# Performance work log

Measured on AMD Instinct MI355X. Metric: run time of the kernel, lower is better.

The kernel has to match this reference:

```python
import jax, jax.numpy as jnp
import numpy as np
from jax import lax

EPS = 1e-5

def conv4d(x, w, stride=1, padding=0):
    # x: [N, C, X, Y, Z, W4]; w: [O, I, kx, ky, kz, kw]
    dn = lax.conv_dimension_numbers(x.shape, w.shape, ('NCXYZW', 'OIXYZW', 'NCXYZW'))
    return lax.conv_general_dilated(x, w, window_strides=(stride,) * 4,
                                    padding=[(padding, padding)] * 4,
                                    dimension_numbers=dn)

def groupnorm1(x, w, b):
    # GroupNorm(num_groups=1): normalize over channel + all spatial dims per sample
    mu = jnp.mean(x, axis=(1, 2, 3, 4, 5), keepdims=True)
    var = jnp.mean(jnp.square(x - mu), axis=(1, 2, 3, 4, 5), keepdims=True)
    xn = (x - mu) * lax.rsqrt(var + EPS)
    shape = (1, -1, 1, 1, 1, 1)
    return xn * w.reshape(shape) + b.reshape(shape)

def setup_inputs() -> dict:
    key = jax.random.key(0)
    ks = jax.random.split(key, 16)
    inp, oup, hidden, se_dim = 32, 32, 128, 8  # hidden = inp*4, se_dim = int(inp*0.25)
    B, S = 1, 16
    sc1 = 1.0 / np.sqrt(inp)
    sc3 = 1.0 / np.sqrt(hidden * 81)
    scp = 1.0 / np.sqrt(hidden)
    return {
        'x': jax.random.normal(ks[0], (B, inp, S, S, S, S), dtype=jnp.float32),
        'g0_w': jnp.ones((inp,), jnp.float32),
        'g0_b': jnp.zeros((inp,), jnp.float32),
        'w1': jax.random.normal(ks[1], (hidden, inp, 1, 1, 1, 1), jnp.float32) * sc1,
        'gn1_w': jnp.ones((hidden,), jnp.float32),
        'gn1_b': jnp.zeros((hidden,), jnp.float32),
        'w2': jax.random.normal(ks[2], (hidden, hidden, 3, 3, 3, 3), jnp.float32) * sc3,
        'gn2_w': jnp.ones((hidden,), jnp.float32),
        'gn2_b': jnp.zeros((hidden,), jnp.float32),
        'se_w1': jax.random.normal(ks[3], (se_dim, hidden), jnp.float32) * scp,
        'se_w2': jax.random.normal(ks[4], (hidden, se_dim), jnp.float32) / np.sqrt(se_dim),
        'w3': jax.random.normal(ks[5], (oup, hidden, 1, 1, 1, 1), jnp.float32) * scp,
        'gn3_w': jnp.ones((oup,), jnp.float32),
        'gn3_b': jnp.zeros((oup,), jnp.float32),
    }

def reference(x, g0_w, g0_b, w1, gn1_w, gn1_b, w2, gn2_w, gn2_b, se_w1, se_w2, w3, gn3_w, gn3_b):
    # PreNorm
    h = groupnorm1(x, g0_w, g0_b)
    # expand 1^4 conv + GN + GELU
    h = conv4d(h, w1)
    h = jax.nn.gelu(groupnorm1(h, gn1_w, gn1_b), approximate=False)
    # 3^4 conv, pad 1 + GN + GELU
    h = conv4d(h, w2, padding=1)
    h = jax.nn.gelu(groupnorm1(h, gn2_w, gn2_b), approximate=False)
    # SE: squeeze over 4 spatial dims, Linear -> GELU -> Linear -> sigmoid, scale
    y = jnp.mean(h, axis=(2, 3, 4, 5))                      # [B, hidden]
    y = jax.nn.gelu(y @ se_w1.T, approximate=False) @ se_w2.T
    y = jax.nn.sigmoid(y)[:, :, None, None, None, None]
    h = h * y
    # project 1^4 conv + GN
    h = conv4d(h, w3)
    return groupnorm1(h, gn3_w, gn3_b)
```

## Files before the change

kernel.cpp:

```cpp
#include <hip/hip_runtime.h>
#include <hip/hip_bf16.h>
#include <math.h>

typedef __hip_bfloat16 bf16;
typedef short bf16x8 __attribute__((ext_vector_type(8)));
typedef float f32x4 __attribute__((ext_vector_type(4)));

#define EPSV 1e-5f

__device__ __forceinline__ float gelu_exact(float x) {
    return 0.5f * x * (1.0f + erff(x * 0.70710678118654752f));
}

__device__ __forceinline__ void block_reduce2(float& a, float& b, float* sm) {
    #pragma unroll
    for (int off = 32; off > 0; off >>= 1) {
        a += __shfl_down(a, off);
        b += __shfl_down(b, off);
    }
    int lane = threadIdx.x & 63, wid = threadIdx.x >> 6;
    int nw = blockDim.x >> 6;
    if (lane == 0) { sm[wid*2] = a; sm[wid*2+1] = b; }
    __syncthreads();
    if (threadIdx.x == 0) {
        for (int i = 1; i < nw; ++i) { a += sm[i*2]; b += sm[i*2+1]; }
    }
}

__device__ __forceinline__ unsigned pk_bf2(float lo, float hi) {
    union { __hip_bfloat162 b2; unsigned u; } cv;
    cv.b2 = __float22bfloat162_rn(make_float2(lo, hi));
    return cv.u;
}

__device__ __forceinline__ void gload_lds16(const void* g, void* l) {
    __builtin_amdgcn_global_load_lds(
        (const __attribute__((address_space(1))) void*)g,
        (__attribute__((address_space(3))) void*)l, 16, 0, 0);
}

__global__ __launch_bounds__(256) void k0_stats_x(const float* __restrict__ x,
                                                  float* __restrict__ stats) {
    __shared__ float sm[16];
    const float4* x4 = (const float4*)x;
    int idx = blockIdx.x * 256 + threadIdx.x;
    float s = 0.f, q = 0.f;
    for (int i = idx; i < (1 << 19); i += gridDim.x * 256) {
        float4 v = x4[i];
        s += v.x + v.y + v.z + v.w;
        q += v.x*v.x + v.y*v.y + v.z*v.z + v.w*v.w;
    }
    block_reduce2(s, q, sm);
    if (threadIdx.x == 0) { atomicAdd(&stats[0], s); atomicAdd(&stats[1], q); }
}

__global__ __launch_bounds__(256) void kw_transpose(const float* __restrict__ w2,
                                                    bf16* __restrict__ wt2) {
    int idx = blockIdx.x * 256 + threadIdx.x;
    if (idx >= 81 * 128 * 128) return;
    int tap = idx >> 14;
    int r = idx & 16383;
    int o = r >> 7;
    int ci = r & 127;
    wt2[idx] = __float2bfloat16(w2[(o * 128 + ci) * 81 + tap]);
}

__global__ __launch_bounds__(256) void k1_conv1(
    const float* __restrict__ x, const float* __restrict__ w1,
    const float* __restrict__ g0w, const float* __restrict__ g0b,
    float* __restrict__ h1, float* __restrict__ stats)
{
    __shared__ float We[128 * 32];
    __shared__ float Be[128];
    __shared__ float sm[16];
    float mu = stats[0] * (1.f / 2097152.f);
    float var = stats[1] * (1.f / 2097152.f) - mu * mu;
    float rs = rsqrtf(var + EPSV);
    int t = threadIdx.x;
    for (int i = t; i < 128 * 32; i += 256) {
        int ci = i & 31;
        We[i] = w1[i] * g0w[ci] * rs;
    }
    if (t < 128) {
        float acc = 0.f;
        for (int ci = 0; ci < 32; ++ci)
            acc += w1[t * 32 + ci] * (g0b[ci] - mu * rs * g0w[ci]);
        Be[t] = acc;
    }
    __syncthreads();
    int s = blockIdx.x * 256 + t;
    float xv[32];
    #pragma unroll
    for (int ci = 0; ci < 32; ++ci) xv[ci] = x[ci * 65536 + s];
    float lsum = 0.f, lsq = 0.f;
    for (int o = 0; o < 128; ++o) {
        float acc = Be[o];
        const float4* wr = (const float4*)&We[o * 32];
        #pragma unroll
        for (int c4 = 0; c4 < 8; ++c4) {
            float4 w = wr[c4];
            acc += w.x * xv[c4*4] + w.y * xv[c4*4+1] + w.z * xv[c4*4+2] + w.w * xv[c4*4+3];
        }
        h1[o * 65536 + s] = acc;
        lsum += acc; lsq += acc * acc;
    }
    block_reduce2(lsum, lsq, sm);
    if (t == 0) { atomicAdd(&stats[2], lsum); atomicAdd(&stats[3], lsq); }
}

__global__ __launch_bounds__(256) void k2_gn1_pad(
    const float* __restrict__ h1, bf16* __restrict__ P, const float* __restrict__ stats,
    const float* __restrict__ gw, const float* __restrict__ gb)
{
    __shared__ float tile[128 * 65];
    float mu = stats[2] * (1.f / 8388608.f);
    float var = stats[3] * (1.f / 8388608.f) - mu * mu;
    float rs = rsqrtf(var + EPSV);
    int t = threadIdx.x;
    int sbase = blockIdx.x * 64;
    for (int p = 0; p < 32; ++p) {
        int idx = p * 256 + t;
        int ci = idx >> 6, sl = idx & 63;
        float v = h1[ci * 65536 + sbase + sl];
        v = (v - mu) * rs * gw[ci] + gb[ci];
        tile[ci * 65 + sl] = gelu_exact(v);
    }
    __syncthreads();
    for (int p = 0; p < 4; ++p) {
        int idx = p * 256 + t;
        int r = idx >> 4, cg = idx & 15;
        int s = sbase + r;
        int w = s & 15, z = (s >> 4) & 15, y = (s >> 8) & 15, xx = s >> 12;
        int prow = (((xx + 1) * 18 + y + 1) * 18 + z + 1) * 18 + w + 1;
        int c0 = cg * 8;
        uint4 u;
        u.x = pk_bf2(tile[(c0+0)*65 + r], tile[(c0+1)*65 + r]);
        u.y = pk_bf2(tile[(c0+2)*65 + r], tile[(c0+3)*65 + r]);
        u.z = pk_bf2(tile[(c0+4)*65 + r], tile[(c0+5)*65 + r]);
        u.w = pk_bf2(tile[(c0+6)*65 + r], tile[(c0+7)*65 + r]);
        *(uint4*)((char*)P + ((size_t)prow * 256 + c0 * 2)) = u;
    }
}

__global__ __launch_bounds__(256) void k3_conv2(
    const bf16* __restrict__ P, const bf16* __restrict__ wt2,
    float* __restrict__ h2, float* __restrict__ stats)
{
    __shared__ __align__(16) short As[23040];
    __shared__ __align__(16) short Ws[16384];
    __shared__ float sm[16];
    int t = threadIdx.x;
    int lane = t & 63, ww = t >> 6;
    int lo = lane & 15, hi = lane >> 4;
    int b = blockIdx.x;
    int X = b >> 5, Y = (b >> 1) & 15, Z0 = (b & 1) * 8;
    int zg = ww >> 1, og = ww & 1;

    int wbase[4], wxor[4];
    #pragma unroll
    for (int n = 0; n < 4; ++n) {
        int row = og * 64 + n * 16 + lo;
        wbase[n] = row << 8;
        wxor[n] = (row & 7) << 4;
    }

    f32x4 acc[4][4];
    #pragma unroll
    for (int m = 0; m < 4; ++m)
        #pragma unroll
        for (int n = 0; n < 4; ++n) acc[m][n] = (f32x4){0.f, 0.f, 0.f, 0.f};

    const char* Pb = (const char*)P;
    const char* Wb = (const char*)wt2;

    for (int kxy = 0; kxy < 9; ++kxy) {
        int kx = kxy / 3, ky = kxy - kx * 3;
        __syncthreads();
        int rowstart = ((X + kx) * 18 + (Y + ky)) * 324 + Z0 * 18;
        const char* gA = Pb + (size_t)rowstart * 256;
        for (int c = ww; c < 45; c += 4) {
            int L = c * 1024 + lane * 16;
            int srcoff = L ^ (((L >> 8) & 7) << 4);
            gload_lds16(gA + srcoff, (char*)As + c * 1024);
        }
        for (int t9 = 0; t9 < 9; ++t9) {
            int kz = t9 / 3, kw = t9 - kz * 3;
            int tap = kxy * 9 + t9;
            __syncthreads();
            const char* gW = Wb + (size_t)tap * 32768;
            for (int c = ww; c < 32; c += 4) {
                int L = c * 1024 + lane * 16;
                int srcoff = L ^ (((L >> 8) & 7) << 4);
                gload_lds16(gW + srcoff, (char*)Ws + c * 1024);
            }
            int abase[4], axor[4];
            #pragma unroll
            for (int m = 0; m < 4; ++m) {
                int row = (zg * 4 + m + kz) * 18 + lo + kw;
                abase[m] = row << 8;
                axor[m] = (row & 7) << 4;
            }
            __syncthreads();
            #pragma unroll
            for (int kk = 0; kk < 4; ++kk) {
                int cb = kk * 64 + hi * 16;
                bf16x8 a[4], bb[4];
                #pragma unroll
                for (int m = 0; m < 4; ++m)
                    a[m] = *(const bf16x8*)((const char*)As + abase[m] + (cb ^ axor[m]));
                #pragma unroll
                for (int n = 0; n < 4; ++n)
                    bb[n] = *(const bf16x8*)((const char*)Ws + wbase[n] + (cb ^ wxor[n]));
                #pragma unroll
                for (int m = 0; m < 4; ++m)
                    #pragma unroll
                    for (int n = 0; n < 4; ++n)
                        acc[m][n] = __builtin_amdgcn_mfma_f32_16x16x32_bf16(
                            a[m], bb[n], acc[m][n], 0, 0, 0);
            }
        }
    }

    float ls = 0.f, lq = 0.f;
    int sXY = (X * 16 + Y) * 16;
    #pragma unroll
    for (int m = 0; m < 4; ++m) {
        int z = Z0 + zg * 4 + m;
        int s = (sXY + z) * 16 + hi * 4;
        #pragma unroll
        for (int n = 0; n < 4; ++n) {
            int o = og * 64 + n * 16 + lo;
            *(f32x4*)(h2 + (size_t)o * 65536 + s) = acc[m][n];
            #pragma unroll
            for (int e = 0; e < 4; ++e) { float v = acc[m][n][e]; ls += v; lq += v * v; }
        }
    }
    __syncthreads();
    block_reduce2(ls, lq, sm);
    if (t == 0) { atomicAdd(&stats[4], ls); atomicAdd(&stats[5], lq); }
}

__global__ __launch_bounds__(256) void k4_gn2_se(
    float* __restrict__ h2, const float* __restrict__ stats,
    const float* __restrict__ gw, const float* __restrict__ gb,
    float* __restrict__ chansum)
{
    __shared__ float sm[4];
    float mu = stats[4] * (1.f / 8388608.f);
    float var = stats[5] * (1.f / 8388608.f) - mu * mu;
    float rs = rsqrtf(var + EPSV);
    int chan = blockIdx.x >> 4, seg = blockIdx.x & 15;
    float w = gw[chan], bb = gb[chan];
    float lsum = 0.f;
    int base = chan * 65536 + seg * 4096;
    for (int k = 0; k < 16; ++k) {
        int i = base + k * 256 + threadIdx.x;
        float v = gelu_exact((h2[i] - mu) * rs * w + bb);
        h2[i] = v;
        lsum += v;
    }
    #pragma unroll
    for (int off = 32; off > 0; off >>= 1) lsum += __shfl_down(lsum, off);
    int lane = threadIdx.x & 63, wid = threadIdx.x >> 6;
    if (lane == 0) sm[wid] = lsum;
    __syncthreads();
    if (threadIdx.x == 0) atomicAdd(&chansum[chan], sm[0] + sm[1] + sm[2] + sm[3]);
}

__global__ void k5_se(const float* __restrict__ chansum,
                      const float* __restrict__ sw1, const float* __restrict__ sw2,
                      float* __restrict__ sescale)
{
    __shared__ float ym[128];
    __shared__ float t1[8];
    int t = threadIdx.x;
    ym[t] = chansum[t] * (1.f / 65536.f);
    __syncthreads();
    if (t < 8) {
        float a = 0.f;
        for (int o = 0; o < 128; ++o) a += sw1[t * 128 + o] * ym[o];
        t1[t] = gelu_exact(a);
    }
    __syncthreads();
    float a = 0.f;
    #pragma unroll
    for (int d = 0; d < 8; ++d) a += sw2[t * 8 + d] * t1[d];
    sescale[t] = 1.f / (1.f + expf(-a));
}

__global__ __launch_bounds__(256) void k6_conv3(
    const float* __restrict__ h2, const float* __restrict__ w3,
    const float* __restrict__ sescale,
    float* __restrict__ h3, float* __restrict__ stats)
{
    __shared__ float We[128 * 32];
    __shared__ float sm[16];
    int t = threadIdx.x;
    for (int i = t; i < 4096; i += 256) {
        int ci = i >> 5, oc = i & 31;
        We[i] = w3[oc * 128 + ci] * sescale[ci];
    }
    __syncthreads();
    int s = blockIdx.x * 256 + t;
    float acc[32];
    #pragma unroll
    for (int j = 0; j < 32; ++j) acc[j] = 0.f;
    for (int ci = 0; ci < 128; ++ci) {
        float hv = h2[ci * 65536 + s];
        const float4* wr = (const float4*)&We[ci * 32];
        #pragma unroll
        for (int j4 = 0; j4 < 8; ++j4) {
            float4 wv = wr[j4];
            acc[j4*4+0] += hv * wv.x; acc[j4*4+1] += hv * wv.y;
            acc[j4*4+2] += hv * wv.z; acc[j4*4+3] += hv * wv.w;
        }
    }
    float ls = 0.f, lq = 0.f;
    #pragma unroll
    for (int j = 0; j < 32; ++j) {
        float v = acc[j];
        h3[j * 65536 + s] = v;
        ls += v; lq += v * v;
    }
    block_reduce2(ls, lq, sm);
    if (t == 0) { atomicAdd(&stats[6], ls); atomicAdd(&stats[7], lq); }
}

__global__ __launch_bounds__(256) void k7_gn3(
    const float* __restrict__ h3, const float* __restrict__ stats,
    const float* __restrict__ gw, const float* __restrict__ gb,
    float* __restrict__ out)
{
    float mu = stats[6] * (1.f / 2097152.f);
    float var = stats[7] * (1.f / 2097152.f) - mu * mu;
    float rs = rsqrtf(var + EPSV);
    int idx = blockIdx.x * 256 + threadIdx.x;
    int c = idx >> 16;
    out[idx] = (h3[idx] - mu) * rs * gw[c] + gb[c];
}

extern "C" void kernel_launch(void* const* d_in, const int* in_sizes, int n_in,
                              void* d_out, int out_size, void* d_ws, size_t ws_size,
                              hipStream_t stream)
{
    const float* x    = (const float*)d_in[0];
    const float* g0w  = (const float*)d_in[1];
    const float* g0b  = (const float*)d_in[2];
    const float* w1   = (const float*)d_in[3];
    const float* gn1w = (const float*)d_in[4];
    const float* gn1b = (const float*)d_in[5];
    const float* w2   = (const float*)d_in[6];
    const float* gn2w = (const float*)d_in[7];
    const float* gn2b = (const float*)d_in[8];
    const float* sw1  = (const float*)d_in[9];
    const float* sw2  = (const float*)d_in[10];
    const float* w3   = (const float*)d_in[11];
    const float* gn3w = (const float*)d_in[12];
    const float* gn3b = (const float*)d_in[13];
    float* out = (float*)d_out;

    char* ws = (char*)d_ws;
    float* stats   = (float*)ws;
    float* chansum = stats + 64;
    float* sescale = stats + 192;
    bf16*  wt2  = (bf16*)(ws + 4096);
    bf16*  P    = (bf16*)(ws + 2658304);
    float* hbuf = (float*)(ws + 29532160);
    float* h3   = (float*)(ws + 63086592);

    hipMemsetAsync(stats, 0, 4096, stream);
    hipMemsetAsync(P, 0, (size_t)104976 * 128 * 2, stream);
    kw_transpose<<<5184, 256, 0, stream>>>(w2, wt2);
    k0_stats_x<<<1024, 256, 0, stream>>>(x, stats);
    k1_conv1<<<256, 256, 0, stream>>>(x, w1, g0w, g0b, hbuf, stats);
    k2_gn1_pad<<<1024, 256, 0, stream>>>(hbuf, P, stats, gn1w, gn1b);
    k3_conv2<<<512, 256, 0, stream>>>(P, wt2, hbuf, stats);
    k4_gn2_se<<<2048, 256, 0, stream>>>(hbuf, stats, gn2w, gn2b, chansum);
    k5_se<<<1, 128, 0, stream>>>(chansum, sw1, sw2, sescale);
    k6_conv3<<<256, 256, 0, stream>>>(hbuf, w3, sescale, h3, stats);
    k7_gn3<<<8192, 256, 0, stream>>>(h3, stats, gn3w, gn3b, out);
}
```

Before: 399.7 us.

## Fuse small kernels, read conv2 weights from global, remap blocks, raise occupancy

Merges the weight transpose and input-stats kernels into one launch, and folds the SE MLP into each conv3 block so the separate single-block SE kernel goes away. In conv2, the per-tap weight staging through LDS, and the two barriers around it for each of the 81 taps, are removed. The MFMA B operands are now loaded straight from global memory (cache-resident bf16 weights), which cuts LDS use and allows the 3-blocks-per-CU launch bound. A block-index swizzle spreads neighbouring tiles across XCDs. The trade-off is more global and cache traffic for weight reads inside the inner MFMA loop, plus redundant SE computation in every conv3 block.

```diff
diff --git a/kernel.cpp b/kernel.cpp
--- a/kernel.cpp
+++ b/kernel.cpp
@@ -39,30 +39,31 @@
         (__attribute__((address_space(3))) void*)l, 16, 0, 0);
 }
 
-__global__ __launch_bounds__(256) void k0_stats_x(const float* __restrict__ x,
-                                                  float* __restrict__ stats) {
+__global__ __launch_bounds__(256) void kw_k0(
+    const float* __restrict__ w2, bf16* __restrict__ wt2,
+    const float* __restrict__ x, float* __restrict__ stats)
+{
     __shared__ float sm[16];
-    const float4* x4 = (const float4*)x;
-    int idx = blockIdx.x * 256 + threadIdx.x;
-    float s = 0.f, q = 0.f;
-    for (int i = idx; i < (1 << 19); i += gridDim.x * 256) {
-        float4 v = x4[i];
-        s += v.x + v.y + v.z + v.w;
-        q += v.x*v.x + v.y*v.y + v.z*v.z + v.w*v.w;
-    }
-    block_reduce2(s, q, sm);
-    if (threadIdx.x == 0) { atomicAdd(&stats[0], s); atomicAdd(&stats[1], q); }
-}
-
-__global__ __launch_bounds__(256) void kw_transpose(const float* __restrict__ w2,
-                                                    bf16* __restrict__ wt2) {
-    int idx = blockIdx.x * 256 + threadIdx.x;
-    if (idx >= 81 * 128 * 128) return;
-    int tap = idx >> 14;
-    int r = idx & 16383;
-    int o = r >> 7;
-    int ci = r & 127;
-    wt2[idx] = __float2bfloat16(w2[(o * 128 + ci) * 81 + tap]);
+    int b = blockIdx.x;
+    if (b < 5184) {
+        int idx = b * 256 + threadIdx.x;
+        int tap = idx >> 14;
+        int r = idx & 16383;
+        int o = r >> 7;
+        int ci = r & 127;
+        wt2[idx] = __float2bfloat16(w2[(o * 128 + ci) * 81 + tap]);
+    } else {
+        const float4* x4 = (const float4*)x;
+        int idx = (b - 5184) * 256 + threadIdx.x;
+        float s = 0.f, q = 0.f;
+        for (int i = idx; i < (1 << 19); i += 1024 * 256) {
+            float4 v = x4[i];
+            s += v.x + v.y + v.z + v.w;
+            q += v.x*v.x + v.y*v.y + v.z*v.z + v.w*v.w;
+        }
+        block_reduce2(s, q, sm);
+        if (threadIdx.x == 0) { atomicAdd(&stats[0], s); atomicAdd(&stats[1], q); }
+    }
 }
 
 __global__ __launch_bounds__(256) void k1_conv1(
@@ -142,36 +143,32 @@
     }
 }
 
-__global__ __launch_bounds__(256) void k3_conv2(
+__global__ __launch_bounds__(256, 3) void k3_conv2(
     const bf16* __restrict__ P, const bf16* __restrict__ wt2,
     float* __restrict__ h2, float* __restrict__ stats)
 {
     __shared__ __align__(16) short As[23040];
-    __shared__ __align__(16) short Ws[16384];
     __shared__ float sm[16];
     int t = threadIdx.x;
     int lane = t & 63, ww = t >> 6;
     int lo = lane & 15, hi = lane >> 4;
-    int b = blockIdx.x;
+    int b = ((blockIdx.x & 7) << 6) | (blockIdx.x >> 3);
     int X = b >> 5, Y = (b >> 1) & 15, Z0 = (b & 1) * 8;
     int zg = ww >> 1, og = ww & 1;
 
-    int wbase[4], wxor[4];
-    #pragma unroll
-    for (int n = 0; n < 4; ++n) {
-        int row = og * 64 + n * 16 + lo;
-        wbase[n] = row << 8;
-        wxor[n] = (row & 7) << 4;
-    }
-
-    f32x4 acc[4][4];
-    #pragma unroll
-    for (int m = 0; m < 4; ++m)
-        #pragma unroll
-        for (int n = 0; n < 4; ++n) acc[m][n] = (f32x4){0.f, 0.f, 0.f, 0.f};
-
     const char* Pb = (const char*)P;
     const char* Wb = (const char*)wt2;
+
+    const char* wbase[4];
+    #pragma unroll
+    for (int n = 0; n < 4; ++n)
+        wbase[n] = Wb + (og * 64 + n * 16 + lo) * 256 + hi * 16;
+
+    f32x4 acc[4][4];
+    #pragma unroll
+    for (int m = 0; m < 4; ++m)
+        #pragma unroll
+        for (int n = 0; n < 4; ++n) acc[m][n] = (f32x4){0.f, 0.f, 0.f, 0.f};
 
     for (int kxy = 0; kxy < 9; ++kxy) {
         int kx = kxy / 3, ky = kxy - kx * 3;
@@ -183,16 +180,12 @@
             int srcoff = L ^ (((L >> 8) & 7) << 4);
             gload_lds16(gA + srcoff, (char*)As + c * 1024);
         }
+        __syncthreads();
+        #pragma unroll
         for (int t9 = 0; t9 < 9; ++t9) {
             int kz = t9 / 3, kw = t9 - kz * 3;
             int tap = kxy * 9 + t9;
-            __syncthreads();
-            const char* gW = Wb + (size_t)tap * 32768;
-            for (int c = ww; c < 32; c += 4) {
-                int L = c * 1024 + lane * 16;
-                int srcoff = L ^ (((L >> 8) & 7) << 4);
-                gload_lds16(gW + srcoff, (char*)Ws + c * 1024);
-            }
+            size_t toff = (size_t)tap * 32768;
             int abase[4], axor[4];
             #pragma unroll
             for (int m = 0; m < 4; ++m) {
@@ -200,7 +193,6 @@
                 abase[m] = row << 8;
                 axor[m] = (row & 7) << 4;
             }
-            __syncthreads();
             #pragma unroll
             for (int kk = 0; kk < 4; ++kk) {
                 int cb = kk * 64 + hi * 16;
@@ -210,7 +202,7 @@
                     a[m] = *(const bf16x8*)((const char*)As + abase[m] + (cb ^ axor[m]));
                 #pragma unroll
                 for (int n = 0; n < 4; ++n)
-                    bb[n] = *(const bf16x8*)((const char*)Ws + wbase[n] + (cb ^ wxor[n]));
+                    bb[n] = *(const bf16x8*)(wbase[n] + toff + kk * 64);
                 #pragma unroll
                 for (int m = 0; m < 4; ++m)
                     #pragma unroll
@@ -267,38 +259,33 @@
     if (threadIdx.x == 0) atomicAdd(&chansum[chan], sm[0] + sm[1] + sm[2] + sm[3]);
 }
 
-__global__ void k5_se(const float* __restrict__ chansum,
-                      const float* __restrict__ sw1, const float* __restrict__ sw2,
-                      float* __restrict__ sescale)
-{
-    __shared__ float ym[128];
-    __shared__ float t1[8];
+__global__ __launch_bounds__(256) void k6_conv3(
+    const float* __restrict__ h2, const float* __restrict__ w3,
+    const float* __restrict__ chansum,
+    const float* __restrict__ sw1, const float* __restrict__ sw2,
+    float* __restrict__ h3, float* __restrict__ stats)
+{
+    __shared__ float We[128 * 32];
+    __shared__ float sesc[128];
+    __shared__ float t1s[8];
+    __shared__ float sm[16];
     int t = threadIdx.x;
-    ym[t] = chansum[t] * (1.f / 65536.f);
-    __syncthreads();
     if (t < 8) {
         float a = 0.f;
-        for (int o = 0; o < 128; ++o) a += sw1[t * 128 + o] * ym[o];
-        t1[t] = gelu_exact(a);
-    }
-    __syncthreads();
-    float a = 0.f;
-    #pragma unroll
-    for (int d = 0; d < 8; ++d) a += sw2[t * 8 + d] * t1[d];
-    sescale[t] = 1.f / (1.f + expf(-a));
-}
-
-__global__ __launch_bounds__(256) void k6_conv3(
-    const float* __restrict__ h2, const float* __restrict__ w3,
-    const float* __restrict__ sescale,
-    float* __restrict__ h3, float* __restrict__ stats)
-{
-    __shared__ float We[128 * 32];
-    __shared__ float sm[16];
-    int t = threadIdx.x;
+        for (int o = 0; o < 128; ++o) a += sw1[t * 128 + o] * chansum[o];
+        t1s[t] = gelu_exact(a * (1.f / 65536.f));
+    }
+    __syncthreads();
+    if (t < 128) {
+        float a = 0.f;
+        #pragma unroll
+        for (int d = 0; d < 8; ++d) a += sw2[t * 8 + d] * t1s[d];
+        sesc[t] = 1.f / (1.f + expf(-a));
+    }
+    __syncthreads();
     for (int i = t; i < 4096; i += 256) {
         int ci = i >> 5, oc = i & 31;
-        We[i] = w3[oc * 128 + ci] * sescale[ci];
+        We[i] = w3[oc * 128 + ci] * sesc[ci];
     }
     __syncthreads();
     int s = blockIdx.x * 256 + t;
@@ -362,7 +349,6 @@
     char* ws = (char*)d_ws;
     float* stats   = (float*)ws;
     float* chansum = stats + 64;
-    float* sescale = stats + 192;
     bf16*  wt2  = (bf16*)(ws + 4096);
     bf16*  P    = (bf16*)(ws + 2658304);
     float* hbuf = (float*)(ws + 29532160);
@@ -370,13 +356,11 @@
 
     hipMemsetAsync(stats, 0, 4096, stream);
     hipMemsetAsync(P, 0, (size_t)104976 * 128 * 2, stream);
-    kw_transpose<<<5184, 256, 0, stream>>>(w2, wt2);
-    k0_stats_x<<<1024, 256, 0, stream>>>(x, stats);
+    kw_k0<<<6208, 256, 0, stream>>>(w2, wt2, x, stats);
     k1_conv1<<<256, 256, 0, stream>>>(x, w1, g0w, g0b, hbuf, stats);
     k2_gn1_pad<<<1024, 256, 0, stream>>>(hbuf, P, stats, gn1w, gn1b);
     k3_conv2<<<512, 256, 0, stream>>>(P, wt2, hbuf, stats);
     k4_gn2_se<<<2048, 256, 0, stream>>>(hbuf, stats, gn2w, gn2b, chansum);
-    k5_se<<<1, 128, 0, stream>>>(chansum, sw1, sw2, sescale);
-    k6_conv3<<<256, 256, 0, stream>>>(hbuf, w3, sescale, h3, stats);
+    k6_conv3<<<256, 256, 0, stream>>>(hbuf, w3, chansum, sw1, sw2, h3, stats);
     k7_gn3<<<8192, 256, 0, stream>>>(h3, stats, gn3w, gn3b, out);
 }
```

After: 747.7 us. 87.1% more time.
